# Kernel tuning notes

Hardware: AMD Instinct MI355X
Metric: run time of the kernel (lower is better)

Reference implementation:

```python
import jax, jax.numpy as jnp
import numpy as np

N_NODES = 100000


def setup_inputs() -> dict:
    key = jax.random.key(0)
    k1, k2, k3, k4, k5 = jax.random.split(key, 5)
    feat = jax.random.normal(k1, (N_NODES, 128), dtype=jnp.float32)
    src = jax.random.randint(k2, (1600000,), 0, N_NODES, dtype=jnp.int32)
    dst = jax.random.randint(k3, (1600000,), 0, N_NODES, dtype=jnp.int32)
    # Xavier-uniform-like weight init
    limit = float(np.sqrt(6.0 / (128 + 128)))
    weight = jax.random.uniform(k4, (128, 128), minval=-limit, maxval=limit, dtype=jnp.float32)
    bias = jax.random.normal(k5, (128,), dtype=jnp.float32) * 0.0  # zeros per reset_parameters
    return {"feat": feat, "src": src, "dst": dst, "weight": weight, "bias": bias}


def reference(feat, src, dst, weight, bias):
    # copy_u/sum: gather source features along edges, scatter-add into destinations
    agg = jax.ops.segment_sum(feat[src], dst, num_segments=N_NODES)  # [N, in_feats]
    rst = agg @ weight  # [N, out_feats]
    # symmetric-ish degree normalization: in_degree^{-0.5}, clamped at 1
    deg = jax.ops.segment_sum(jnp.ones_like(dst, dtype=feat.dtype), dst, num_segments=N_NODES)
    norm = jnp.clip(deg, 1.0, None) ** -0.5  # [N]
    rst = rst * norm[:, None] + bias
    return rst
```

## Files before the change

### kernel.cpp

```cpp
#include <hip/hip_runtime.h>
#include <hip/hip_bf16.h>

#define CHUNK 1024
#define RR 64
#define PDEPTH 96
#define NSUB 16
#define CAPE 2560
#define SUBWMAX 128
typedef unsigned int uint;
typedef unsigned short ushort;

typedef __bf16 bf16x8 __attribute__((ext_vector_type(8)));
typedef float  f32x4  __attribute__((ext_vector_type(4)));

__device__ __forceinline__ ushort f2bf(float f) {
    const uint u = __float_as_uint(f);
    return (ushort)((u + 0x7fffu + ((u >> 16) & 1u)) >> 16);
}

__global__ __launch_bounds__(256) void partition64(const int* __restrict__ src,
                                                   const int* __restrict__ dst,
                                                   int* __restrict__ gcur,
                                                   uint* __restrict__ staging,
                                                   int cap, int nE, int N) {
    __shared__ uint bins[RR][PDEPTH];
    __shared__ int cnt[RR];
    __shared__ int res[RR];
    const int t  = threadIdx.x;
    const int nb = gridDim.x;
    const int rounds = (nE + nb * 1024 - 1) / (nb * 1024);

    for (int rd = 0; rd < rounds; ++rd) {
        if (t < RR) cnt[t] = 0;
        __syncthreads();

        const int e4 = (rd * nb + blockIdx.x) * 1024 + t * 4;
        int s[4], d[4];
        int nv = 0;
        if (e4 + 3 < nE) {
            const int4 s4 = *reinterpret_cast<const int4*>(src + e4);
            const int4 d4 = *reinterpret_cast<const int4*>(dst + e4);
            s[0] = s4.x; s[1] = s4.y; s[2] = s4.z; s[3] = s4.w;
            d[0] = d4.x; d[1] = d4.y; d[2] = d4.z; d[3] = d4.w;
            nv = 4;
        } else {
            for (int e = e4; e < nE; ++e) { s[nv] = src[e]; d[nv] = dst[e]; ++nv; }
        }
#pragma unroll
        for (int i = 0; i < 4; ++i) {
            if (i < nv) {
                const int r  = (int)(((long long)d[i] * RR) / N);
                const int lo = (int)(((long long)r * N + RR - 1) / RR);
                const uint pk = (uint)s[i] | ((uint)(d[i] - lo) << 17);
                const int pos = atomicAdd(&cnt[r], 1);
                if (pos < PDEPTH) {
                    bins[r][pos] = pk;
                } else {
                    const int gp = atomicAdd(&gcur[r], 1);
                    staging[(size_t)r * cap + gp] = pk;
                }
            }
        }
        __syncthreads();
        if (t < RR) {
            int c = cnt[t];
            c = c < PDEPTH ? c : PDEPTH;
            cnt[t] = c;
            res[t] = (c > 0) ? atomicAdd(&gcur[t], c) : 0;
        }
        __syncthreads();
        {
            const int w    = t >> 6;
            const int lane = t & 63;
            for (int rr = w * 16; rr < w * 16 + 16; ++rr) {
                const int c = cnt[rr];
                const int b = res[rr];
                uint* sp = staging + (size_t)rr * cap + b;
                if (lane < c) sp[lane] = bins[rr][lane];
                if (c > 64 && lane + 64 < c) sp[64 + lane] = bins[rr][64 + lane];
            }
        }
        __syncthreads();
    }
}

__global__ __launch_bounds__(256) void prep_w(const float* __restrict__ w,
                                              ushort* __restrict__ wt,
                                              int* __restrict__ gcur) {
    if (blockIdx.x == 0 && threadIdx.x < RR) gcur[threadIdx.x] = 0;
    const int idx = blockIdx.x * 256 + threadIdx.x;
    const int k = idx >> 7;
    const int n = idx & 127;
    wt[n * 128 + k] = f2bf(w[k * 128 + n]);
}

#define APITCH 136
__global__ __launch_bounds__(256, 4) void gemm_mfma(const float* __restrict__ feat,
                                                    const ushort* __restrict__ wt,
                                                    ushort* __restrict__ h, int M) {
    __shared__ ushort A_lds[64 * APITCH];
    const int t    = threadIdx.x;
    const int wave = t >> 6;
    const int lane = t & 63;
    const int quad = lane >> 4;
    const int nn   = lane & 15;
    const int row0 = blockIdx.x * 64;

#pragma unroll
    for (int p = 0; p < 8; ++p) {
        const int idx = p * 256 + t;
        const int row = idx >> 5;
        const int c4  = (idx & 31) * 4;
        const int grow = row0 + row;
        float4 v = make_float4(0.f, 0.f, 0.f, 0.f);
        if (grow < M)
            v = *reinterpret_cast<const float4*>(&feat[(size_t)grow * 128 + c4]);
        const uint2 pk = make_uint2((uint)f2bf(v.x) | ((uint)f2bf(v.y) << 16),
                                    (uint)f2bf(v.z) | ((uint)f2bf(v.w) << 16));
        *reinterpret_cast<uint2*>(&A_lds[row * APITCH + c4]) = pk;
    }
    __syncthreads();

    union UA { uint4 u; bf16x8 b; };
    union UB { uint4 u; bf16x8 b; };
    UA afrag[4];
#pragma unroll
    for (int kc = 0; kc < 4; ++kc)
        afrag[kc].u = *reinterpret_cast<const uint4*>(
            &A_lds[(wave * 16 + nn) * APITCH + kc * 32 + quad * 8]);

    f32x4 acc[8];
#pragma unroll
    for (int ct = 0; ct < 8; ++ct) {
        UB bfr[4];
#pragma unroll
        for (int kc = 0; kc < 4; ++kc)
            bfr[kc].u = *reinterpret_cast<const uint4*>(
                wt + (ct * 16 + nn) * 128 + kc * 32 + quad * 8);
        acc[ct] = (f32x4){0.f, 0.f, 0.f, 0.f};
#pragma unroll
        for (int kc = 0; kc < 4; ++kc)
            acc[ct] = __builtin_amdgcn_mfma_f32_16x16x32_bf16(
                afrag[kc].b, bfr[kc].b, acc[ct], 0, 0, 0);
    }
    __syncthreads();

#pragma unroll
    for (int ct = 0; ct < 8; ++ct) {
#pragma unroll
        for (int reg = 0; reg < 4; ++reg) {
            const int rl = wave * 16 + quad * 4 + reg;
            A_lds[rl * APITCH + ct * 16 + nn] = f2bf(acc[ct][reg]);
        }
    }
    __syncthreads();

#pragma unroll
    for (int p = 0; p < 4; ++p) {
        const int idx = p * 256 + t;
        const int row = idx >> 4;
        const int c16 = idx & 15;
        const int grow = row0 + row;
        if (grow < M) {
            const uint4 v = *reinterpret_cast<const uint4*>(&A_lds[row * APITCH + c16 * 8]);
            *reinterpret_cast<uint4*>(&h[(size_t)grow * 128 + c16 * 8]) = v;
        }
    }
}

__global__ __launch_bounds__(512, 4) void build_agg(const uint* __restrict__ staging,
                                                    const int* __restrict__ gcur,
                                                    const ushort* __restrict__ h,
                                                    const float* __restrict__ bias,
                                                    float* __restrict__ out, int cap, int N) {
    __shared__ uint epack[CAPE];
    __shared__ int  csr_s[CAPE];
    __shared__ int  hist[SUBWMAX];
    __shared__ int  off_s[SUBWMAX];
    __shared__ int  cur_s[SUBWMAX];
    __shared__ int  sbuf[SUBWMAX];
    __shared__ int  scnt;

    const int t    = threadIdx.x;
    const int bid  = blockIdx.x;
    const int xcd  = bid & 7;
    const int i2   = bid >> 3;
    const int r    = xcd * 8 + (i2 >> 4);
    const int sub  = i2 & (NSUB - 1);

    const int lo   = (int)(((long long)r * N + RR - 1) / RR);
    const int hi   = (int)(((long long)(r + 1) * N + RR - 1) / RR);
    const int W    = hi - lo;
    const int SUBW = (W + NSUB - 1) / NSUB;
    const int nlo  = sub * SUBW;
    const int nhi  = min(W, nlo + SUBW);
    const int SW   = nhi - nlo;
    if (SW <= 0) return;

    const int  cnt_r = gcur[r];
    const uint* ep   = staging + (size_t)r * cap;
    const int  lane  = t & 63;

    if (t == 0) scnt = 0;
    if (t < SUBWMAX) hist[t] = 0;
    __syncthreads();

    const int nall = (cnt_r + 511) & ~511;
    for (int i = t; i < nall; i += 512) {
        uint v = 0;
        bool keep = false;
        if (i < cnt_r) {
            v = ep[i];
            const int ld = (int)(v >> 17);
            keep = (ld >= nlo) && (ld < nhi);
        }
        const unsigned long long m = __ballot(keep);
        const int tot = __popcll(m);
        if (tot) {
            int wb = 0;
            if (lane == 0) wb = atomicAdd(&scnt, tot);
            wb = __shfl(wb, 0);
            if (keep) {
                const int p = wb + __popcll(m & ((1ull << lane) - 1ull));
                if (p < CAPE) epack[p] = v;
            }
        }
    }
    __syncthreads();
    const int ne = min(scnt, CAPE);

    for (int i = t; i < ne; i += 512)
        atomicAdd(&hist[(int)(epack[i] >> 17) - nlo], 1);
    __syncthreads();

    int v0 = 0;
    if (t < SUBWMAX) { v0 = hist[t]; sbuf[t] = v0; }
    __syncthreads();
    for (int d = 1; d < SUBWMAX; d <<= 1) {
        int x = 0;
        if (t < SUBWMAX && t >= d) x = sbuf[t - d];
        __syncthreads();
        if (t < SUBWMAX) sbuf[t] += x;
        __syncthreads();
    }
    if (t < SUBWMAX) { const int e = sbuf[t] - v0; off_s[t] = e; cur_s[t] = e; }
    __syncthreads();

    for (int i = t; i < ne; i += 512) {
        const uint v  = epack[i];
        const int ld  = (int)(v >> 17) - nlo;
        const int pos = atomicAdd(&cur_s[ld], 1);
        csr_s[pos] = (int)(v & 0x1FFFFu);
    }
    __syncthreads();

    const int wv  = t >> 6;
    const int q   = lane >> 4;
    const int sbl = lane & 15;

#define UNPACK_ADD(rr)                                             \
    do {                                                           \
        acc[0] += __uint_as_float(((rr).x & 0xffffu) << 16);       \
        acc[1] += __uint_as_float((rr).x & 0xffff0000u);           \
        acc[2] += __uint_as_float(((rr).y & 0xffffu) << 16);       \
        acc[3] += __uint_as_float((rr).y & 0xffff0000u);           \
        acc[4] += __uint_as_float(((rr).z & 0xffffu) << 16);       \
        acc[5] += __uint_as_float((rr).z & 0xffff0000u);           \
        acc[6] += __uint_as_float(((rr).w & 0xffffu) << 16);       \
        acc[7] += __uint_as_float((rr).w & 0xffff0000u);           \
    } while (0)

    for (int n = wv; n < SW; n += 8) {
        const int start = off_s[n];
        const int dg    = hist[n];
        const int end   = start + dg;

        float acc[8];
#pragma unroll
        for (int k = 0; k < 8; ++k) acc[k] = 0.0f;

        int j = start;
        for (; j + 15 < end; j += 16) {
            int s[4];
#pragma unroll
            for (int k = 0; k < 4; ++k) s[k] = csr_s[j + q + 4 * k];
            uint4 rg[4];
#pragma unroll
            for (int k = 0; k < 4; ++k)
                rg[k] = *reinterpret_cast<const uint4*>(h + (size_t)s[k] * 128 + sbl * 8);
#pragma unroll
            for (int k = 0; k < 4; ++k) UNPACK_ADD(rg[k]);
        }
        for (; j + 3 < end; j += 4) {
            const int s = csr_s[j + q];
            const uint4 rr = *reinterpret_cast<const uint4*>(h + (size_t)s * 128 + sbl * 8);
            UNPACK_ADD(rr);
        }
        const int rem = end - j;
        if (q < rem) {
            const int s = csr_s[j + q];
            const uint4 rr = *reinterpret_cast<const uint4*>(h + (size_t)s * 128 + sbl * 8);
            UNPACK_ADD(rr);
        }

#pragma unroll
        for (int k = 0; k < 8; ++k) {
            acc[k] += __shfl_xor(acc[k], 16, 64);
            acc[k] += __shfl_xor(acc[k], 32, 64);
        }

        if (lane < 16) {
            const float nm = rsqrtf(fmaxf((float)dg, 1.0f));
            const float4 b0 = *reinterpret_cast<const float4*>(bias + sbl * 8 + 0);
            const float4 b1 = *reinterpret_cast<const float4*>(bias + sbl * 8 + 4);
            float4 o0, o1;
            o0.x = fmaf(acc[0], nm, b0.x);
            o0.y = fmaf(acc[1], nm, b0.y);
            o0.z = fmaf(acc[2], nm, b0.z);
            o0.w = fmaf(acc[3], nm, b0.w);
            o1.x = fmaf(acc[4], nm, b1.x);
            o1.y = fmaf(acc[5], nm, b1.y);
            o1.z = fmaf(acc[6], nm, b1.z);
            o1.w = fmaf(acc[7], nm, b1.w);
            const size_t gnode = (size_t)(lo + nlo + n);
            *reinterpret_cast<float4*>(out + gnode * 128 + sbl * 8 + 0) = o0;
            *reinterpret_cast<float4*>(out + gnode * 128 + sbl * 8 + 4) = o1;
        }
    }
#undef UNPACK_ADD
}

__global__ void hist_simple(const int* __restrict__ dst, int* __restrict__ deg, int nE) {
    int e = blockIdx.x * blockDim.x + threadIdx.x;
    if (e < nE) atomicAdd(&deg[dst[e]], 1);
}
__global__ void bucket_simple(const int* __restrict__ src, const int* __restrict__ dst,
                              int* __restrict__ cur, int* __restrict__ csr, int nE) {
    int e = blockIdx.x * blockDim.x + threadIdx.x;
    if (e < nE) {
        int pos = atomicAdd(&cur[dst[e]], 1);
        csr[pos] = src[e];
    }
}
__global__ __launch_bounds__(256) void scan_chunks(const int* __restrict__ deg,
                                                   int* __restrict__ off,
                                                   int* __restrict__ partials, int N) {
    __shared__ int sums[256];
    const int b = blockIdx.x, t = threadIdx.x;
    const int base = b * CHUNK + t * 4;
    int v[4];
#pragma unroll
    for (int i = 0; i < 4; ++i) v[i] = (base + i < N) ? deg[base + i] : 0;
    const int s = v[0] + v[1] + v[2] + v[3];
    sums[t] = s;
    __syncthreads();
    for (int d = 1; d < 256; d <<= 1) {
        int x = (t >= d) ? sums[t - d] : 0;
        __syncthreads();
        sums[t] += x;
        __syncthreads();
    }
    const int excl = sums[t] - s;
    if (t == 255) partials[b] = sums[255];
    int run = excl;
#pragma unroll
    for (int i = 0; i < 4; ++i) {
        if (base + i < N) off[base + i] = run;
        run += v[i];
    }
}
__global__ __launch_bounds__(256) void scan_partials(int* partials, int P) {
    __shared__ int buf[256];
    const int t = threadIdx.x;
    if (P <= 256) {
        const int v = (t < P) ? partials[t] : 0;
        buf[t] = v;
        __syncthreads();
        for (int d = 1; d < 256; d <<= 1) {
            int x = (t >= d) ? buf[t - d] : 0;
            __syncthreads();
            buf[t] += x;
            __syncthreads();
        }
        if (t < P) partials[t] = buf[t] - v;
    } else if (t == 0) {
        int acc = 0;
        for (int i = 0; i < P; ++i) { int v = partials[i]; partials[i] = acc; acc += v; }
    }
}
__global__ void add_base(int* __restrict__ off, int* __restrict__ cur,
                         const int* __restrict__ partials, int N) {
    int i = blockIdx.x * blockDim.x + threadIdx.x;
    if (i < N) {
        int o = off[i] + partials[i >> 10];
        off[i] = o;
        cur[i] = o;
    }
}
__global__ __launch_bounds__(256) void aggregate_f32(const float* __restrict__ feat,
                                                     const int* __restrict__ csr,
                                                     const int* __restrict__ off,
                                                     const int* __restrict__ deg,
                                                     float* __restrict__ out, int N) {
    const int node = (blockIdx.x * blockDim.x + threadIdx.x) >> 6;
    if (node >= N) return;
    const int lane = threadIdx.x & 63;
    const int start = off[node];
    const int end   = start + deg[node];
    const float2* feat2 = reinterpret_cast<const float2*>(feat);
    float ax = 0.0f, ay = 0.0f;
    for (int j = start; j < end; ++j) {
        const float2 v = feat2[(size_t)csr[j] * 64 + lane];
        ax += v.x;
        ay += v.y;
    }
    reinterpret_cast<float2*>(out)[(size_t)node * 64 + lane] = make_float2(ax, ay);
}
__global__ __launch_bounds__(256) void gemm_norm(const float* agg,
                                                 const float* __restrict__ weight,
                                                 const float* __restrict__ bias,
                                                 const int* __restrict__ deg,
                                                 float* out, int M) {
    __shared__ float As[64][68];
    __shared__ float Wc[64][128];
    const int t  = threadIdx.x;
    const int tx = t & 15;
    const int ty = t >> 4;
    const int row0 = blockIdx.x * 64;
    float acc[4][8];
#pragma unroll
    for (int i = 0; i < 4; ++i)
#pragma unroll
        for (int j = 0; j < 8; ++j) acc[i][j] = 0.0f;
    for (int c = 0; c < 2; ++c) {
        if (c) __syncthreads();
        {
            const int k4 = (t & 15) * 4;
            const int rbase = t >> 4;
#pragma unroll
            for (int p = 0; p < 4; ++p) {
                const int rr = rbase + p * 16;
                const int grow = row0 + rr;
                float4 v = make_float4(0.f, 0.f, 0.f, 0.f);
                if (grow < M)
                    v = *reinterpret_cast<const float4*>(&agg[(size_t)grow * 128 + c * 64 + k4]);
                *reinterpret_cast<float4*>(&As[rr][k4]) = v;
            }
        }
        {
#pragma unroll
            for (int p = 0; p < 8; ++p) {
                const int idx = (p * 256 + t) * 4;
                const int kk = idx >> 7;
                const int j = idx & 127;
                *reinterpret_cast<float4*>(&Wc[kk][j]) =
                    *reinterpret_cast<const float4*>(&weight[(c * 64 + kk) * 128 + j]);
            }
        }
        __syncthreads();
#pragma unroll 8
        for (int k = 0; k < 64; ++k) {
            float a[4];
#pragma unroll
            for (int i = 0; i < 4; ++i) a[i] = As[ty * 4 + i][k];
            const float4 b0 = *reinterpret_cast<const float4*>(&Wc[k][tx * 8 + 0]);
            const float4 b1 = *reinterpret_cast<const float4*>(&Wc[k][tx * 8 + 4]);
            const float b[8] = {b0.x, b0.y, b0.z, b0.w, b1.x, b1.y, b1.z, b1.w};
#pragma unroll
            for (int i = 0; i < 4; ++i)
#pragma unroll
                for (int j = 0; j < 8; ++j)
                    acc[i][j] = fmaf(a[i], b[j], acc[i][j]);
        }
    }
    float bcol[8];
#pragma unroll
    for (int j = 0; j < 8; ++j) bcol[j] = bias[tx * 8 + j];
#pragma unroll
    for (int i = 0; i < 4; ++i) {
        const int grow = row0 + ty * 4 + i;
        if (grow < M) {
            const float nm = rsqrtf(fmaxf((float)deg[grow], 1.0f));
            float4 o0, o1;
            o0.x = fmaf(acc[i][0], nm, bcol[0]);
            o0.y = fmaf(acc[i][1], nm, bcol[1]);
            o0.z = fmaf(acc[i][2], nm, bcol[2]);
            o0.w = fmaf(acc[i][3], nm, bcol[3]);
            o1.x = fmaf(acc[i][4], nm, bcol[4]);
            o1.y = fmaf(acc[i][5], nm, bcol[5]);
            o1.z = fmaf(acc[i][6], nm, bcol[6]);
            o1.w = fmaf(acc[i][7], nm, bcol[7]);
            *reinterpret_cast<float4*>(&out[(size_t)grow * 128 + tx * 8 + 0]) = o0;
            *reinterpret_cast<float4*>(&out[(size_t)grow * 128 + tx * 8 + 4]) = o1;
        }
    }
}

extern "C" void kernel_launch(void* const* d_in, const int* in_sizes, int n_in,
                              void* d_out, int out_size, void* d_ws, size_t ws_size,
                              hipStream_t stream) {
    const float* feat   = (const float*)d_in[0];
    const int*   src    = (const int*)d_in[1];
    const int*   dst    = (const int*)d_in[2];
    const float* weight = (const float*)d_in[3];
    const float* bias   = (const float*)d_in[4];
    float* out = (float*)d_out;

    const int nE = in_sizes[1];
    const int M  = in_sizes[0] / 128;
    const int P  = (M + CHUNK - 1) / CHUNK;

    int*    gcur    = (int*)d_ws;
    ushort* wt      = (ushort*)(gcur + RR);
    uint*   staging = (uint*)(wt + 16384);
    const int cap = (((nE + RR - 1) / RR + 8192) + 3) & ~3;
    ushort* h = (ushort*)(staging + (size_t)RR * cap);
    const size_t need = (size_t)RR * 4 + 32768 + (size_t)RR * cap * 4 + (size_t)M * 128 * 2;

    if (ws_size >= need && M <= 131072) {
        prep_w<<<64, 256, 0, stream>>>(weight, wt, gcur);
        gemm_mfma<<<(M + 63) / 64, 256, 0, stream>>>(feat, wt, h, M);
        partition64<<<1024, 256, 0, stream>>>(src, dst, gcur, staging, cap, nE, M);
        build_agg<<<RR * NSUB, 512, 0, stream>>>(staging, gcur, h, bias, out, cap, M);
    } else {
        int* degi     = (int*)d_ws;
        int* off      = degi + M;
        int* cur      = off + M;
        int* partials = cur + M;
        int* csr      = partials + 256;
        hipMemsetAsync(degi, 0, (size_t)M * sizeof(int), stream);
        hist_simple<<<(nE + 255) / 256, 256, 0, stream>>>(dst, degi, nE);
        scan_chunks<<<P, 256, 0, stream>>>(degi, off, partials, M);
        scan_partials<<<1, 256, 0, stream>>>(partials, P);
        add_base<<<(M + 255) / 256, 256, 0, stream>>>(off, cur, partials, M);
        bucket_simple<<<(nE + 255) / 256, 256, 0, stream>>>(src, dst, cur, csr, nE);
        aggregate_f32<<<(M + 3) / 4, 256, 0, stream>>>(feat, csr, off, degi, out, M);
        gemm_norm<<<(M + 63) / 64, 256, 0, stream>>>(out, weight, bias, degi, out, M);
    }
}
```

Measured before the change: 253.4 us.

## Fuse weight prep, GEMM and edge partition into one interleaved kernel

```diff
diff --git a/kernel.cpp b/kernel.cpp
--- a/kernel.cpp
+++ b/kernel.cpp
@@ -18,157 +18,169 @@
     return (ushort)((u + 0x7fffu + ((u >> 16) & 1u)) >> 16);
 }
 
-__global__ __launch_bounds__(256) void partition64(const int* __restrict__ src,
-                                                   const int* __restrict__ dst,
-                                                   int* __restrict__ gcur,
-                                                   uint* __restrict__ staging,
-                                                   int cap, int nE, int N) {
-    __shared__ uint bins[RR][PDEPTH];
-    __shared__ int cnt[RR];
-    __shared__ int res[RR];
-    const int t  = threadIdx.x;
-    const int nb = gridDim.x;
-    const int rounds = (nE + nb * 1024 - 1) / (nb * 1024);
-
-    for (int rd = 0; rd < rounds; ++rd) {
-        if (t < RR) cnt[t] = 0;
-        __syncthreads();
-
-        const int e4 = (rd * nb + blockIdx.x) * 1024 + t * 4;
-        int s[4], d[4];
-        int nv = 0;
-        if (e4 + 3 < nE) {
-            const int4 s4 = *reinterpret_cast<const int4*>(src + e4);
-            const int4 d4 = *reinterpret_cast<const int4*>(dst + e4);
-            s[0] = s4.x; s[1] = s4.y; s[2] = s4.z; s[3] = s4.w;
-            d[0] = d4.x; d[1] = d4.y; d[2] = d4.z; d[3] = d4.w;
-            nv = 4;
-        } else {
-            for (int e = e4; e < nE; ++e) { s[nv] = src[e]; d[nv] = dst[e]; ++nv; }
-        }
-#pragma unroll
-        for (int i = 0; i < 4; ++i) {
-            if (i < nv) {
-                const int r  = (int)(((long long)d[i] * RR) / N);
-                const int lo = (int)(((long long)r * N + RR - 1) / RR);
-                const uint pk = (uint)s[i] | ((uint)(d[i] - lo) << 17);
-                const int pos = atomicAdd(&cnt[r], 1);
-                if (pos < PDEPTH) {
-                    bins[r][pos] = pk;
-                } else {
-                    const int gp = atomicAdd(&gcur[r], 1);
-                    staging[(size_t)r * cap + gp] = pk;
+#define APITCH 136
+#define WPITCH 132
+#define SMEM_BYTES (128 * WPITCH * 2 + 64 * APITCH * 2)
+
+__global__ __launch_bounds__(256, 3) void gemm_part(const float* __restrict__ feat,
+                                                    const float* __restrict__ weight,
+                                                    const int* __restrict__ src,
+                                                    const int* __restrict__ dst,
+                                                    int* __restrict__ gcur,
+                                                    uint* __restrict__ staging,
+                                                    ushort* __restrict__ h,
+                                                    int cap, int nE, int M) {
+    __shared__ __align__(16) char smem[SMEM_BYTES];
+    const int t    = threadIdx.x;
+    const int kind = blockIdx.x & 1;
+    const int idx  = blockIdx.x >> 1;
+
+    if (kind == 0) {
+        const int row0 = idx * 64;
+        if (row0 >= M) return;
+        ushort* W_lds = (ushort*)smem;
+        ushort* A_lds = (ushort*)(smem + 128 * WPITCH * 2);
+        const int wave = t >> 6;
+        const int lane = t & 63;
+        const int quad = lane >> 4;
+        const int nn   = lane & 15;
+
+#pragma unroll
+        for (int p = 0; p < 16; ++p) {
+            const int ii = p * 256 + t;
+            const int k  = ii >> 5;
+            const int n4 = (ii & 31) * 4;
+            const float4 w4 = *reinterpret_cast<const float4*>(weight + k * 128 + n4);
+            W_lds[(n4 + 0) * WPITCH + k] = f2bf(w4.x);
+            W_lds[(n4 + 1) * WPITCH + k] = f2bf(w4.y);
+            W_lds[(n4 + 2) * WPITCH + k] = f2bf(w4.z);
+            W_lds[(n4 + 3) * WPITCH + k] = f2bf(w4.w);
+        }
+
+#pragma unroll
+        for (int p = 0; p < 8; ++p) {
+            const int ii  = p * 256 + t;
+            const int row = ii >> 5;
+            const int c4  = (ii & 31) * 4;
+            const int grow = row0 + row;
+            float4 v = make_float4(0.f, 0.f, 0.f, 0.f);
+            if (grow < M)
+                v = *reinterpret_cast<const float4*>(&feat[(size_t)grow * 128 + c4]);
+            const uint2 pk = make_uint2((uint)f2bf(v.x) | ((uint)f2bf(v.y) << 16),
+                                        (uint)f2bf(v.z) | ((uint)f2bf(v.w) << 16));
+            *reinterpret_cast<uint2*>(&A_lds[row * APITCH + c4]) = pk;
+        }
+        __syncthreads();
+
+        union UA { uint4 u; bf16x8 b; };
+        union UB { uint4 u; bf16x8 b; };
+        UA afrag[4];
+#pragma unroll
+        for (int kc = 0; kc < 4; ++kc)
+            afrag[kc].u = *reinterpret_cast<const uint4*>(
+                &A_lds[(wave * 16 + nn) * APITCH + kc * 32 + quad * 8]);
+
+        f32x4 acc[8];
+#pragma unroll
+        for (int ct = 0; ct < 8; ++ct) {
+            UB bfr[4];
+#pragma unroll
+            for (int kc = 0; kc < 4; ++kc)
+                bfr[kc].u = *reinterpret_cast<const uint4*>(
+                    &W_lds[(ct * 16 + nn) * WPITCH + kc * 32 + quad * 8]);
+            acc[ct] = (f32x4){0.f, 0.f, 0.f, 0.f};
+#pragma unroll
+            for (int kc = 0; kc < 4; ++kc)
+                acc[ct] = __builtin_amdgcn_mfma_f32_16x16x32_bf16(
+                    afrag[kc].b, bfr[kc].b, acc[ct], 0, 0, 0);
+        }
+        __syncthreads();
+
+#pragma unroll
+        for (int ct = 0; ct < 8; ++ct) {
+#pragma unroll
+            for (int reg = 0; reg < 4; ++reg) {
+                const int rl = wave * 16 + quad * 4 + reg;
+                A_lds[rl * APITCH + ct * 16 + nn] = f2bf(acc[ct][reg]);
+            }
+        }
+        __syncthreads();
+
+#pragma unroll
+        for (int p = 0; p < 4; ++p) {
+            const int ii  = p * 256 + t;
+            const int row = ii >> 4;
+            const int c16 = ii & 15;
+            const int grow = row0 + row;
+            if (grow < M) {
+                const uint4 v = *reinterpret_cast<const uint4*>(&A_lds[row * APITCH + c16 * 8]);
+                *reinterpret_cast<uint4*>(&h[(size_t)grow * 128 + c16 * 8]) = v;
+            }
+        }
+    } else {
+        uint (*bins)[PDEPTH] = (uint(*)[PDEPTH])smem;
+        int* cnt = (int*)(smem + RR * PDEPTH * 4);
+        int* res = cnt + RR;
+        const int nb = gridDim.x >> 1;
+        const int N  = M;
+        const int rounds = (nE + nb * 1024 - 1) / (nb * 1024);
+
+        for (int rd = 0; rd < rounds; ++rd) {
+            if (t < RR) cnt[t] = 0;
+            __syncthreads();
+
+            const int e4 = (rd * nb + idx) * 1024 + t * 4;
+            int s[4], d[4];
+            int nv = 0;
+            if (e4 + 3 < nE) {
+                const int4 s4 = *reinterpret_cast<const int4*>(src + e4);
+                const int4 d4 = *reinterpret_cast<const int4*>(dst + e4);
+                s[0] = s4.x; s[1] = s4.y; s[2] = s4.z; s[3] = s4.w;
+                d[0] = d4.x; d[1] = d4.y; d[2] = d4.z; d[3] = d4.w;
+                nv = 4;
+            } else {
+                for (int e = e4; e < nE; ++e) { s[nv] = src[e]; d[nv] = dst[e]; ++nv; }
+            }
+#pragma unroll
+            for (int i = 0; i < 4; ++i) {
+                if (i < nv) {
+                    const int r  = (int)(((long long)d[i] * RR) / N);
+                    const int lo = (int)(((long long)r * N + RR - 1) / RR);
+                    const uint pk = (uint)s[i] | ((uint)(d[i] - lo) << 17);
+                    const int pos = atomicAdd(&cnt[r], 1);
+                    if (pos < PDEPTH) {
+                        bins[r][pos] = pk;
+                    } else {
+                        const int gp = atomicAdd(&gcur[r], 1);
+                        staging[(size_t)r * cap + gp] = pk;
+                    }
                 }
             }
-        }
-        __syncthreads();
-        if (t < RR) {
-            int c = cnt[t];
-            c = c < PDEPTH ? c : PDEPTH;
-            cnt[t] = c;
-            res[t] = (c > 0) ? atomicAdd(&gcur[t], c) : 0;
-        }
-        __syncthreads();
-        {
-            const int w    = t >> 6;
-            const int lane = t & 63;
-            for (int rr = w * 16; rr < w * 16 + 16; ++rr) {
-                const int c = cnt[rr];
-                const int b = res[rr];
-                uint* sp = staging + (size_t)rr * cap + b;
-                if (lane < c) sp[lane] = bins[rr][lane];
-                if (c > 64 && lane + 64 < c) sp[64 + lane] = bins[rr][64 + lane];
-            }
-        }
-        __syncthreads();
-    }
-}
-
-__global__ __launch_bounds__(256) void prep_w(const float* __restrict__ w,
-                                              ushort* __restrict__ wt,
-                                              int* __restrict__ gcur) {
-    if (blockIdx.x == 0 && threadIdx.x < RR) gcur[threadIdx.x] = 0;
-    const int idx = blockIdx.x * 256 + threadIdx.x;
-    const int k = idx >> 7;
-    const int n = idx & 127;
-    wt[n * 128 + k] = f2bf(w[k * 128 + n]);
-}
-
-#define APITCH 136
-__global__ __launch_bounds__(256, 4) void gemm_mfma(const float* __restrict__ feat,
-                                                    const ushort* __restrict__ wt,
-                                                    ushort* __restrict__ h, int M) {
-    __shared__ ushort A_lds[64 * APITCH];
-    const int t    = threadIdx.x;
-    const int wave = t >> 6;
-    const int lane = t & 63;
-    const int quad = lane >> 4;
-    const int nn   = lane & 15;
-    const int row0 = blockIdx.x * 64;
-
-#pragma unroll
-    for (int p = 0; p < 8; ++p) {
-        const int idx = p * 256 + t;
-        const int row = idx >> 5;
-        const int c4  = (idx & 31) * 4;
-        const int grow = row0 + row;
-        float4 v = make_float4(0.f, 0.f, 0.f, 0.f);
-        if (grow < M)
-            v = *reinterpret_cast<const float4*>(&feat[(size_t)grow * 128 + c4]);
-        const uint2 pk = make_uint2((uint)f2bf(v.x) | ((uint)f2bf(v.y) << 16),
-                                    (uint)f2bf(v.z) | ((uint)f2bf(v.w) << 16));
-        *reinterpret_cast<uint2*>(&A_lds[row * APITCH + c4]) = pk;
-    }
-    __syncthreads();
-
-    union UA { uint4 u; bf16x8 b; };
-    union UB { uint4 u; bf16x8 b; };
-    UA afrag[4];
-#pragma unroll
-    for (int kc = 0; kc < 4; ++kc)
-        afrag[kc].u = *reinterpret_cast<const uint4*>(
-            &A_lds[(wave * 16 + nn) * APITCH + kc * 32 + quad * 8]);
-
-    f32x4 acc[8];
-#pragma unroll
-    for (int ct = 0; ct < 8; ++ct) {
-        UB bfr[4];
-#pragma unroll
-        for (int kc = 0; kc < 4; ++kc)
-            bfr[kc].u = *reinterpret_cast<const uint4*>(
-                wt + (ct * 16 + nn) * 128 + kc * 32 + quad * 8);
-        acc[ct] = (f32x4){0.f, 0.f, 0.f, 0.f};
-#pragma unroll
-        for (int kc = 0; kc < 4; ++kc)
-            acc[ct] = __builtin_amdgcn_mfma_f32_16x16x32_bf16(
-                afrag[kc].b, bfr[kc].b, acc[ct], 0, 0, 0);
-    }
-    __syncthreads();
-
-#pragma unroll
-    for (int ct = 0; ct < 8; ++ct) {
-#pragma unroll
-        for (int reg = 0; reg < 4; ++reg) {
-            const int rl = wave * 16 + quad * 4 + reg;
-            A_lds[rl * APITCH + ct * 16 + nn] = f2bf(acc[ct][reg]);
-        }
-    }
-    __syncthreads();
-
-#pragma unroll
-    for (int p = 0; p < 4; ++p) {
-        const int idx = p * 256 + t;
-        const int row = idx >> 4;
-        const int c16 = idx & 15;
-        const int grow = row0 + row;
-        if (grow < M) {
-            const uint4 v = *reinterpret_cast<const uint4*>(&A_lds[row * APITCH + c16 * 8]);
-            *reinterpret_cast<uint4*>(&h[(size_t)grow * 128 + c16 * 8]) = v;
-        }
-    }
-}
-
-__global__ __launch_bounds__(512, 4) void build_agg(const uint* __restrict__ staging,
+            __syncthreads();
+            if (t < RR) {
+                int c = cnt[t];
+                c = c < PDEPTH ? c : PDEPTH;
+                cnt[t] = c;
+                res[t] = (c > 0) ? atomicAdd(&gcur[t], c) : 0;
+            }
+            __syncthreads();
+            {
+                const int w    = t >> 6;
+                const int lane = t & 63;
+                for (int rr = w * 16; rr < w * 16 + 16; ++rr) {
+                    const int c = cnt[rr];
+                    const int b = res[rr];
+                    uint* sp = staging + (size_t)rr * cap + b;
+                    if (lane < c) sp[lane] = bins[rr][lane];
+                    if (c > 64 && lane + 64 < c) sp[64 + lane] = bins[rr][64 + lane];
+                }
+            }
+            __syncthreads();
+        }
+    }
+}
+
+__global__ __launch_bounds__(512, 8) void build_agg(const uint* __restrict__ staging,
                                                     const int* __restrict__ gcur,
                                                     const ushort* __restrict__ h,
                                                     const float* __restrict__ bias,
@@ -511,16 +523,18 @@
     const int P  = (M + CHUNK - 1) / CHUNK;
 
     int*    gcur    = (int*)d_ws;
-    ushort* wt      = (ushort*)(gcur + RR);
-    uint*   staging = (uint*)(wt + 16384);
+    uint*   staging = (uint*)(gcur + RR);
     const int cap = (((nE + RR - 1) / RR + 8192) + 3) & ~3;
     ushort* h = (ushort*)(staging + (size_t)RR * cap);
-    const size_t need = (size_t)RR * 4 + 32768 + (size_t)RR * cap * 4 + (size_t)M * 128 * 2;
-
-    if (ws_size >= need && M <= 131072) {
-        prep_w<<<64, 256, 0, stream>>>(weight, wt, gcur);
-        gemm_mfma<<<(M + 63) / 64, 256, 0, stream>>>(feat, wt, h, M);
-        partition64<<<1024, 256, 0, stream>>>(src, dst, gcur, staging, cap, nE, M);
+    const size_t need = (size_t)RR * 4 + (size_t)RR * cap * 4 + (size_t)M * 128 * 2;
+
+    if (ws_size >= need && M <= 102400) {
+        const int gblocks = (M + 63) / 64;
+        const int pblocks = 1600;
+        const int half    = gblocks > pblocks ? gblocks : pblocks;
+        hipMemsetAsync(gcur, 0, RR * sizeof(int), stream);
+        gemm_part<<<2 * half, 256, 0, stream>>>(feat, weight, src, dst,
+                                                gcur, staging, h, cap, nE, M);
         build_agg<<<RR * NSUB, 512, 0, stream>>>(staging, gcur, h, bias, out, cap, M);
     } else {
         int* degi     = (int*)d_ws;
```

Result: slower. 259.9 us (+2.6%).
